# Kernel optimization log

Measured on AMD Instinct MI355X. Metric: run time of the kernel, lower is better.

Reference implementation:

```python
import jax, jax.numpy as jnp
import numpy as np

IMG = 224      # img_size
P = 16         # patch_size
C = 3          # in_chans
K = 100        # n_segments
COMPACT = 10.0 # slic compactness
ITERS = 10     # slic k-means iterations


def _resize_matrix(src, dst):
    # Linear antialiased resize is a linear map; materialize it by resizing identity.
    return jax.image.resize(jnp.eye(src, dtype=jnp.float32), (dst, src),
                            method='linear', antialias=True)


def _slic_labels(img_hwc):
    """Simplified SLIC: grid-initialized k-means in (color, compactness-scaled xy) space."""
    H, W = IMG, IMG
    S = float(np.sqrt(H * W / K))         # superpixel spacing
    ratio = COMPACT / S                   # spatial scaling (SLIC distance weighting)
    yy, xx = jnp.meshgrid(jnp.arange(H, dtype=jnp.float32),
                          jnp.arange(W, dtype=jnp.float32), indexing='ij')
    feat = jnp.concatenate([img_hwc, (yy * ratio)[..., None], (xx * ratio)[..., None]],
                           axis=-1).reshape(H * W, C + 2)  # [HW, 5]
    # grid init of K centers
    gh = int(np.ceil(np.sqrt(K)))
    gw = int(np.ceil(K / gh))
    cy = ((np.arange(gh) + 0.5) * H / gh).astype(np.int32)
    cx = ((np.arange(gw) + 0.5) * W / gw).astype(np.int32)
    idx = (cy[:, None] * W + cx[None, :]).reshape(-1)[:K]
    centers0 = feat[jnp.asarray(idx)]  # [K, 5]

    f2 = jnp.sum(feat * feat, axis=1, keepdims=True)  # [HW,1]

    def dists(centers):
        c2 = jnp.sum(centers * centers, axis=1)  # [K]
        return f2 + c2[None, :] - 2.0 * (feat @ centers.T)  # [HW,K]

    def body(i, centers):
        lbl = jnp.argmin(dists(centers), axis=1)              # [HW]
        oh = jax.nn.one_hot(lbl, K, dtype=feat.dtype)         # [HW,K]
        cnt = oh.sum(0)                                       # [K]
        new = (oh.T @ feat) / jnp.maximum(cnt, 1.0)[:, None]  # [K,5]
        return jnp.where((cnt > 0)[:, None], new, centers)

    centers = jax.lax.fori_loop(0, ITERS, body, centers0)
    return jnp.argmin(dists(centers), axis=1).reshape(H, W)


def _embed_one(img_chw, A):
    img = jnp.transpose(img_chw, (1, 2, 0))                     # [H,W,C]
    labels = jax.lax.stop_gradient(_slic_labels(img))           # [H,W] int
    masks = jax.nn.one_hot(labels, K, dtype=img.dtype, axis=0)  # [K,H,W]
    masked = masks[..., None] * img[None]                       # [K,H,W,C]
    tmp = jnp.einsum('ph,khwc->kpwc', A, masked)                # resize rows
    return jnp.einsum('qw,kpwc->kpqc', A, tmp)                  # [K,P,P,C]


def reference(x):
    B = x.shape[0]
    A = _resize_matrix(IMG, P)
    sp = jax.vmap(lambda im: _embed_one(im, A))(x)  # [B,K,P,P,C]
    # torch: view(B, K*C, P, P)  (raw row-major reinterpret), flatten(2), transpose(1,2)
    out = sp.reshape(B, K * C, P, P).reshape(B, K * C, P * P)
    return jnp.transpose(out, (0, 2, 1))  # [B, P*P, K*C]


def setup_inputs() -> dict:
    key = jax.random.key(0)
    x = jax.random.uniform(key, (8, C, IMG, IMG), dtype=jnp.float32)
    return {"x": x}
```

## Files before the change

### kernel.cpp

```cpp
#include <hip/hip_runtime.h>
#include <math.h>

#define IMGD 224
#define HW 50176
#define NK 100
#define NB 8
#define OUT_PER_B 76800
#define NCHUNK 131
#define MSTR 13
#define PSLAB 640


static __device__ __forceinline__ float ratio_f32() {
  return (float)(10.0 / sqrt(224.0 * 224.0 / 100.0));
}

static __device__ __forceinline__ float dist5s(float f0, float f1, float f2,
                                               float f3, float f4, float fsq,
                                               float c0, float c1, float c2,
                                               float c3, float c4, float q) {
  float dot = __fmul_rn(f0, c0);
  dot = __fmaf_rn(f1, c1, dot);
  dot = __fmaf_rn(f2, c2, dot);
  dot = __fmaf_rn(f3, c3, dot);
  dot = __fmaf_rn(f4, c4, dot);
  return __fsub_rn(__fadd_rn(fsq, q), __fmul_rn(2.0f, dot));
}

static __device__ __forceinline__ float fsq5(float f0, float f1, float f2,
                                             float f3, float f4) {
  float s = __fmul_rn(f0, f0);
  s = __fadd_rn(s, __fmul_rn(f1, f1));
  s = __fadd_rn(s, __fmul_rn(f2, f2));
  s = __fadd_rn(s, __fmul_rn(f3, f3));
  s = __fadd_rn(s, __fmul_rn(f4, f4));
  return s;
}

__global__ void __launch_bounds__(256, 4) iter_kernel(
    const float* __restrict__ x, float* __restrict__ centers,
    const float* __restrict__ c2g, float* __restrict__ partials, int flag,
    float* __restrict__ Ag) {
  __shared__ float4 ck4[NK];
  __shared__ float2 ck2[NK];
  __shared__ unsigned int maskS[2][NK * MSTR];
  __shared__ unsigned short ppkS[2][NK * MSTR];
  __shared__ float4 cval4[2][384];
  __shared__ float  cvalf[2][384];
  __shared__ int cntS[2][128];
  __shared__ int offxS[2][128];
  __shared__ int wtotS[2];
  __shared__ float ubpart[2][12][10];
  __shared__ float ubg[2][12];
  __shared__ unsigned int candm[2][12][4];
  __shared__ float ared[128];
  int bx = blockIdx.x, b = blockIdx.y;
  int tid = threadIdx.x;

  if (bx >= 66) {
    for (int rr = 0; rr < 2; ++rr) {
      int p = 2 * b + rr;
      float cp = (p + 0.5f) * 14.0f - 0.5f;
      if (tid < 128) {
        float xd0 = fabsf(cp - (float)tid) / 14.0f;
        float trip0 = fmaxf(0.0f, 1.0f - xd0);
        float trip1 = 0.0f;
        int t2 = tid + 128;
        if (t2 < IMGD) {
          float xd = fabsf(cp - (float)t2) / 14.0f;
          trip1 = fmaxf(0.0f, 1.0f - xd);
        }
        ared[tid] = trip0 + trip1;
      }
      __syncthreads();
      for (int s = 64; s > 0; s >>= 1) {
        if (tid < s) ared[tid] += ared[tid + s];
        __syncthreads();
      }
      float Zp = ared[0];
      __syncthreads();
      if (tid < IMGD) {
        float xd = fabsf(cp - (float)tid) / 14.0f;
        Ag[p * IMGD + tid] = fmaxf(0.0f, 1.0f - xd) / Zp;
      }
      __syncthreads();
    }
    return;
  }

  int half = tid >> 7;
  int lt = tid & 127;
  int c = 2 * bx + half;
  int start, len;
  if (c < NCHUNK) {
    start = (c < 129) ? c * 384 : 49536 + (c - 129) * 320;
    len   = (c < 129) ? 384 : 320;
  } else {
    start = 0; len = 0;
  }

  const float ratio = ratio_f32();
  const float* x0 = x + (size_t)b * 3 * HW;
  if (flag == 0) {
    if (tid < NK) {
      int gy = tid / 10, gx = tid - 10 * (tid / 10);
      int cy = (int)((gy + 0.5) * 224.0 / 10.0);
      int cx = (int)((gx + 0.5) * 224.0 / 10.0);
      int i = cy * IMGD + cx;
      float c0 = x0[i], c1 = x0[HW + i], c2 = x0[2 * HW + i];
      float c3 = __fmul_rn((float)cy, ratio);
      float c4 = __fmul_rn((float)cx, ratio);
      float s = __fmul_rn(c0, c0);
      s = __fadd_rn(s, __fmul_rn(c1, c1));
      s = __fadd_rn(s, __fmul_rn(c2, c2));
      s = __fadd_rn(s, __fmul_rn(c3, c3));
      s = __fadd_rn(s, __fmul_rn(c4, c4));
      ck4[tid] = make_float4(c0, c1, c2, c3);
      ck2[tid] = make_float2(c4, s);
      if (bx == 0) {
        float* oc = centers + ((size_t)b * NK + tid) * 5;
        oc[0] = c0; oc[1] = c1; oc[2] = c2; oc[3] = c3; oc[4] = c4;
      }
    }
  } else {
    const float* cb = centers + (size_t)b * NK * 5;
    const float* c2b = c2g + (size_t)b * NK;
    if (tid < NK) {
      ck4[tid] = make_float4(cb[tid*5+0], cb[tid*5+1], cb[tid*5+2], cb[tid*5+3]);
      ck2[tid] = make_float2(cb[tid*5+4], c2b[tid]);
    }
  }
  for (int t = lt; t < NK * MSTR; t += 128) maskS[half][t] = 0u;
  if (lt < 48) candm[half][lt >> 2][lt & 3] = 0u;

  float f0[3], f1[3], f2[3], f3[3], f4[3], fq[3];
  bool vld[3];
  for (int r = 0; r < 3; ++r) {
    int t = lt + r * 128;
    vld[r] = (t < len);
    int i = start + (vld[r] ? t : 0);
    int y = i / IMGD, xw = i - y * IMGD;
    f0[r] = x0[i]; f1[r] = x0[HW + i]; f2[r] = x0[2 * HW + i];
    f3[r] = __fmul_rn((float)y, ratio);
    f4[r] = __fmul_rn((float)xw, ratio);
    fq[r] = fsq5(f0[r], f1[r], f2[r], f3[r], f4[r]);
  }
  __syncthreads();

  if (lt < 120) {
    int g = lt / 10, kb = lt - 10 * g;
    int i0 = start + g * 32, i1 = i0 + 31;
    int ymin = i0 / IMGD, ymax = i1 / IMGD;
    int cmin = (ymin == ymax) ? (i0 - ymin * IMGD) : 0;
    int cmax = (ymin == ymax) ? (i1 - ymax * IMGD) : (IMGD - 1);
    float f3mn = __fmul_rn((float)ymin, ratio);
    float f3mx = __fmul_rn((float)ymax, ratio);
    float f4mn = __fmul_rn((float)cmin, ratio);
    float f4mx = __fmul_rn((float)cmax, ratio);
    float mn = 3.4e38f;
    for (int k = kb * 10; k < kb * 10 + 10; ++k) {
      float c3 = ck4[k].w, c4 = ck2[k].x;
      float dy = fmaxf(fabsf(c3 - f3mn), fabsf(c3 - f3mx));
      float dx = fmaxf(fabsf(c4 - f4mn), fabsf(c4 - f4mx));
      mn = fminf(mn, dy * dy + dx * dx + 3.0f);
    }
    ubpart[half][g][kb] = mn;
  }
  __syncthreads();
  if (lt < 12) {
    float mn = ubpart[half][lt][0];
    for (int j = 1; j < 10; ++j) mn = fminf(mn, ubpart[half][lt][j]);
    ubg[half][lt] = mn + 1.0f;
  }
  __syncthreads();
  if (lt < 120) {
    int g = lt / 10, kb = lt - 10 * g;
    int i0 = start + g * 32, i1 = i0 + 31;
    int ymin = i0 / IMGD, ymax = i1 / IMGD;
    int cmin = (ymin == ymax) ? (i0 - ymin * IMGD) : 0;
    int cmax = (ymin == ymax) ? (i1 - ymax * IMGD) : (IMGD - 1);
    float f3mn = __fmul_rn((float)ymin, ratio);
    float f3mx = __fmul_rn((float)ymax, ratio);
    float f4mn = __fmul_rn((float)cmin, ratio);
    float f4mx = __fmul_rn((float)cmax, ratio);
    float lim = ubg[half][g];
    for (int k = kb * 10; k < kb * 10 + 10; ++k) {
      float c3 = ck4[k].w, c4 = ck2[k].x;
      float dy = fmaxf(0.0f, fmaxf(f3mn - c3, c3 - f3mx));
      float dx = fmaxf(0.0f, fmaxf(f4mn - c4, c4 - f4mx));
      if (dy * dy + dx * dx <= lim)
        atomicOr(&candm[half][g][k >> 5], 1u << (k & 31));
    }
  }
  __syncthreads();

  float best[3]; int bk[3];
  for (int r = 0; r < 3; ++r) {
    best[r] = 3.4e38f; bk[r] = 0;
    int t = lt + r * 128;
    int g = (t < 384) ? (t >> 5) : 0;
    for (int w = 0; w < 4; ++w) {
      unsigned int m = candm[half][g][w];
      while (m) {
        int j = __ffs(m) - 1;
        m &= m - 1;
        int k = (w << 5) + j;
        float4 a4 = ck4[k];
        float2 a2 = ck2[k];
        float d = dist5s(f0[r], f1[r], f2[r], f3[r], f4[r], fq[r],
                         a4.x, a4.y, a4.z, a4.w, a2.x, a2.y);
        if (d < best[r]) { best[r] = d; bk[r] = k; }
      }
    }
  }
  for (int r = 0; r < 3; ++r) {
    int t = lt + r * 128;
    if (vld[r]) atomicOr(&maskS[half][bk[r] * MSTR + (t >> 5)], 1u << (t & 31));
  }
  __syncthreads();

  int myCnt = 0;
  if (lt < NK) {
    int s = 0;
    for (int g = 0; g < 12; ++g) {
      ppkS[half][lt * MSTR + g] = (unsigned short)s;
      s += __popc(maskS[half][lt * MSTR + g]);
    }
    myCnt = s;
  }
  cntS[half][lt] = myCnt;
  __syncthreads();

  int v = myCnt;
  for (int d = 1; d < 64; d <<= 1) {
    int u = __shfl_up(v, d, 64);
    if ((tid & 63) >= d) v += u;
  }
  if (lt == 63) wtotS[half] = v;
  __syncthreads();
  if (lt >= 64) v += wtotS[half];
  offxS[half][lt] = v;
  __syncthreads();

  for (int r = 0; r < 3; ++r) {
    int t = lt + r * 128;
    if (vld[r]) {
      int g = t >> 5, j = t & 31;
      unsigned int m = maskS[half][bk[r] * MSTR + g];
      int rank = ppkS[half][bk[r] * MSTR + g] + __popc(m & ((1u << j) - 1u));
      int pos = offxS[half][bk[r]] - cntS[half][bk[r]] + rank;
      cval4[half][pos] = make_float4(f0[r], f1[r], f2[r], f3[r]);
      cvalf[half][pos] = f4[r];
    }
  }
  __syncthreads();

  if (c < NCHUNK && lt < NK) {
    int n = cntS[half][lt];
    int base = offxS[half][lt] - n;
    float s0 = 0.f, s1 = 0.f, s2 = 0.f, s3 = 0.f, s4 = 0.f, s5 = 0.f;
    for (int m = 0; m < n; ++m) {
      float4 vv = cval4[half][base + m];
      float ww = cvalf[half][base + m];
      s0 = __fadd_rn(s0, vv.x);
      s1 = __fadd_rn(s1, vv.y);
      s2 = __fadd_rn(s2, vv.z);
      s3 = __fadd_rn(s3, vv.w);
      s4 = __fadd_rn(s4, ww);
      s5 += 1.0f;
    }
    float* pp = partials + ((size_t)(b * NCHUNK + c)) * PSLAB + lt * 6;
    pp[0] = s0; pp[1] = s1; pp[2] = s2; pp[3] = s3; pp[4] = s4; pp[5] = s5;
  }
}

__global__ void __launch_bounds__(256) combine_update_kernel(
    float* __restrict__ centers, const float* __restrict__ partials,
    float* __restrict__ c2g) {
  __shared__ float st[8 * 6 * NCHUNK];
  __shared__ float sums[8][6];
  __shared__ float newc[8][5];
  int bb = blockIdx.x;
  int tid = threadIdx.x;
  for (int t = tid; t < 8 * 6 * NCHUNK; t += 256) {
    int c = t / 48;
    int rr = t - 48 * c;
    int row = bb * 8 + rr / 6;
    int comp = rr - 6 * (rr / 6);
    int bi = row / 100, ki = row - 100 * bi;
    st[rr * NCHUNK + c] =
        partials[((size_t)(bi * NCHUNK + c)) * PSLAB + ki * 6 + comp];
  }
  __syncthreads();
  if (tid < 48) {
    int row = tid / 6, comp = tid - 6 * (tid / 6);
    const float* rp = st + (row * 6 + comp) * NCHUNK;
    float s = rp[0];
    for (int c = 1; c < NCHUNK; ++c) s = __fadd_rn(s, rp[c]);
    sums[row][comp] = s;
  }
  __syncthreads();
  if (tid < 40) {
    int row = tid / 5, d = tid - 5 * (tid / 5);
    float cntv = sums[row][5];
    float* cc = centers + (size_t)(bb * 8 + row) * 5;
    float v;
    if (cntv > 0.0f) {
      float m = fmaxf(cntv, 1.0f);
      v = __fdiv_rn(sums[row][d], m);
      cc[d] = v;
    } else {
      v = cc[d];
    }
    newc[row][d] = v;
  }
  __syncthreads();
  if (tid < 8) {
    float t0 = __fmul_rn(newc[tid][0], newc[tid][0]);
    t0 = __fadd_rn(t0, __fmul_rn(newc[tid][1], newc[tid][1]));
    t0 = __fadd_rn(t0, __fmul_rn(newc[tid][2], newc[tid][2]));
    t0 = __fadd_rn(t0, __fmul_rn(newc[tid][3], newc[tid][3]));
    t0 = __fadd_rn(t0, __fmul_rn(newc[tid][4], newc[tid][4]));
    c2g[bb * 8 + tid] = t0;
  }
}

__global__ void __launch_bounds__(128, 4) label_kernel(
    const float* __restrict__ x, const float* __restrict__ centers,
    const float* __restrict__ c2g, unsigned char* __restrict__ labels) {
  __shared__ float4 ck4[NK];
  __shared__ float2 ck2[NK];
  __shared__ float ubpart[12][10];
  __shared__ float ubg[12];
  __shared__ unsigned int candm[12][4];
  int c = blockIdx.x, b = blockIdx.y;
  int tid = threadIdx.x;
  int start = (c < 129) ? c * 384 : 49536 + (c - 129) * 320;
  int len   = (c < 129) ? 384 : 320;

  const float ratio = ratio_f32();
  const float* x0 = x + (size_t)b * 3 * HW;
  const float* cb = centers + (size_t)b * NK * 5;
  const float* c2b = c2g + (size_t)b * NK;
  if (tid < NK) {
    ck4[tid] = make_float4(cb[tid*5+0], cb[tid*5+1], cb[tid*5+2], cb[tid*5+3]);
    ck2[tid] = make_float2(cb[tid*5+4], c2b[tid]);
  }
  if (tid < 48) candm[tid >> 2][tid & 3] = 0u;

  float f0[3], f1[3], f2[3], f3[3], f4[3], fq[3];
  int ii[3];
  bool vld[3];
  for (int r = 0; r < 3; ++r) {
    int t = tid + r * 128;
    vld[r] = (t < len);
    int i = start + (vld[r] ? t : 0);
    ii[r] = i;
    int y = i / IMGD, xw = i - y * IMGD;
    f0[r] = x0[i]; f1[r] = x0[HW + i]; f2[r] = x0[2 * HW + i];
    f3[r] = __fmul_rn((float)y, ratio);
    f4[r] = __fmul_rn((float)xw, ratio);
    fq[r] = fsq5(f0[r], f1[r], f2[r], f3[r], f4[r]);
  }
  __syncthreads();

  if (tid < 120) {
    int g = tid / 10, kb = tid - 10 * g;
    int i0 = start + g * 32, i1 = i0 + 31;
    int ymin = i0 / IMGD, ymax = i1 / IMGD;
    int cmin = (ymin == ymax) ? (i0 - ymin * IMGD) : 0;
    int cmax = (ymin == ymax) ? (i1 - ymax * IMGD) : (IMGD - 1);
    float f3mn = __fmul_rn((float)ymin, ratio);
    float f3mx = __fmul_rn((float)ymax, ratio);
    float f4mn = __fmul_rn((float)cmin, ratio);
    float f4mx = __fmul_rn((float)cmax, ratio);
    float mn = 3.4e38f;
    for (int k = kb * 10; k < kb * 10 + 10; ++k) {
      float c3 = ck4[k].w, c4 = ck2[k].x;
      float dy = fmaxf(fabsf(c3 - f3mn), fabsf(c3 - f3mx));
      float dx = fmaxf(fabsf(c4 - f4mn), fabsf(c4 - f4mx));
      mn = fminf(mn, dy * dy + dx * dx + 3.0f);
    }
    ubpart[g][kb] = mn;
  }
  __syncthreads();
  if (tid < 12) {
    float mn = ubpart[tid][0];
    for (int j = 1; j < 10; ++j) mn = fminf(mn, ubpart[tid][j]);
    ubg[tid] = mn + 1.0f;
  }
  __syncthreads();
  if (tid < 120) {
    int g = tid / 10, kb = tid - 10 * g;
    int i0 = start + g * 32, i1 = i0 + 31;
    int ymin = i0 / IMGD, ymax = i1 / IMGD;
    int cmin = (ymin == ymax) ? (i0 - ymin * IMGD) : 0;
    int cmax = (ymin == ymax) ? (i1 - ymax * IMGD) : (IMGD - 1);
    float f3mn = __fmul_rn((float)ymin, ratio);
    float f3mx = __fmul_rn((float)ymax, ratio);
    float f4mn = __fmul_rn((float)cmin, ratio);
    float f4mx = __fmul_rn((float)cmax, ratio);
    float lim = ubg[g];
    for (int k = kb * 10; k < kb * 10 + 10; ++k) {
      float c3 = ck4[k].w, c4 = ck2[k].x;
      float dy = fmaxf(0.0f, fmaxf(f3mn - c3, c3 - f3mx));
      float dx = fmaxf(0.0f, fmaxf(f4mn - c4, c4 - f4mx));
      if (dy * dy + dx * dx <= lim)
        atomicOr(&candm[g][k >> 5], 1u << (k & 31));
    }
  }
  __syncthreads();

  float best[3]; int bk[3];
  for (int r = 0; r < 3; ++r) {
    best[r] = 3.4e38f; bk[r] = 0;
    int t = tid + r * 128;
    int g = (t < 384) ? (t >> 5) : 0;
    for (int w = 0; w < 4; ++w) {
      unsigned int m = candm[g][w];
      while (m) {
        int j = __ffs(m) - 1;
        m &= m - 1;
        int k = (w << 5) + j;
        float4 a4 = ck4[k];
        float2 a2 = ck2[k];
        float d = dist5s(f0[r], f1[r], f2[r], f3[r], f4[r], fq[r],
                         a4.x, a4.y, a4.z, a4.w, a2.x, a2.y);
        if (d < best[r]) { best[r] = d; bk[r] = k; }
      }
    }
  }
  unsigned char* lb = labels + (size_t)b * HW;
  for (int r = 0; r < 3; ++r)
    if (vld[r]) lb[ii[r]] = (unsigned char)bk[r];
}

__global__ void __launch_bounds__(256) embed_kernel(
    const float* __restrict__ x, const unsigned char* __restrict__ labels,
    const float* __restrict__ Ag, float* __restrict__ out) {
  __shared__ float Apv[28];
  __shared__ float Aqw[4][28];
  __shared__ float sk[4][NK * 3];
  int b = blockIdx.y;
  int p = blockIdx.x >> 2;
  int qg = blockIdx.x & 3;
  int q0 = qg * 4;
  int tid = threadIdx.x;

  int h0 = max(0, 14 * p - 7), h1 = min(IMGD - 1, 14 * p + 20);
  int hl = h1 - h0 + 1;
  int w0q[4], w1q[4];
#pragma unroll
  for (int qi = 0; qi < 4; ++qi) {
    int q = q0 + qi;
    w0q[qi] = max(0, 14 * q - 7);
    w1q[qi] = min(IMGD - 1, 14 * q + 20);
  }
  int W0 = w0q[0], W1 = w1q[3];
  int WU = W1 - W0 + 1;

  if (tid < hl) Apv[tid] = Ag[p * IMGD + h0 + tid];
  {
    int t = tid - 64;
    if (t >= 0 && t < 112) {
      int qi = t / 28, dw = t - 28 * qi;
      if (dw <= w1q[qi] - w0q[qi])
        Aqw[qi][dw] = Ag[(q0 + qi) * IMGD + w0q[qi] + dw];
    }
  }
  for (int t = tid; t < 4 * NK * 3; t += 256)
    sk[t / (NK * 3)][t % (NK * 3)] = 0.0f;
  __syncthreads();

  const float* xb = x + (size_t)b * 3 * HW;
  const unsigned char* lb = labels + (size_t)b * HW;
  int n = hl * WU;
  for (int r = 0; r < 8; ++r) {
    int idx = tid + r * 256;
    if (idx >= n) break;
    int dh = idx / WU;
    int dcol = idx - dh * WU;
    int col = W0 + dcol;
    int i = (h0 + dh) * IMGD + col;
    float v0 = xb[i], v1 = xb[HW + i], v2 = xb[2 * HW + i];
    int k = lb[i];
    float ap = Apv[dh];
#pragma unroll
    for (int qi = 0; qi < 4; ++qi) {
      if (col >= w0q[qi] && col <= w1q[qi]) {
        float wgt = ap * Aqw[qi][col - w0q[qi]];
        atomicAdd(&sk[qi][k * 3 + 0], wgt * v0);
        atomicAdd(&sk[qi][k * 3 + 1], wgt * v1);
        atomicAdd(&sk[qi][k * 3 + 2], wgt * v2);
      }
    }
  }
  __syncthreads();

  float* outb = out + (size_t)b * OUT_PER_B;
  for (int t = tid; t < 4 * NK * 3; t += 256) {
    int qi = t / (NK * 3), t3 = t - qi * (NK * 3);
    int k = t3 / 3, cc = t3 - 3 * k;
    int base = p * 48 + (q0 + qi) * 3;
    int f = k * 768 + base + cc;
    outb[(f & 255) * 300 + (f >> 8)] = sk[qi][t3];
  }
}

extern "C" void kernel_launch(void* const* d_in, const int* in_sizes, int n_in,
                              void* d_out, int out_size, void* d_ws, size_t ws_size,
                              hipStream_t stream) {
  const float* x = (const float*)d_in[0];
  float* out = (float*)d_out;
  char* ws = (char*)d_ws;
  float* centers        = (float*)(ws + 16384);
  float* c2g            = (float*)(ws + 49152);
  float* Ag             = (float*)(ws + 65536);
  unsigned char* labels = (unsigned char*)(ws + 98304);
  float* partials       = (float*)(ws + 1703936);

  dim3 ig0(67, NB);
  dim3 ig(66, NB);
  iter_kernel<<<ig0, 256, 0, stream>>>(x, centers, c2g, partials, 0, Ag);
  combine_update_kernel<<<NB * NK / 8, 256, 0, stream>>>(centers, partials, c2g);
  for (int it = 1; it < 10; ++it) {
    iter_kernel<<<ig, 256, 0, stream>>>(x, centers, c2g, partials, 1, Ag);
    combine_update_kernel<<<NB * NK / 8, 256, 0, stream>>>(centers, partials, c2g);
  }
  label_kernel<<<dim3(NCHUNK, NB), 128, 0, stream>>>(x, centers, c2g, labels);
  dim3 egrid(64, NB);
  embed_kernel<<<egrid, 256, 0, stream>>>(x, labels, Ag, out);
}
```

Baseline: 303.7 us.

## Fuse center update into iteration kernels with ping-pong centers and partials buffers

```diff
diff --git a/kernel.cpp b/kernel.cpp
--- a/kernel.cpp
+++ b/kernel.cpp
@@ -38,9 +38,9 @@
 }
 
 __global__ void __launch_bounds__(256, 4) iter_kernel(
-    const float* __restrict__ x, float* __restrict__ centers,
-    const float* __restrict__ c2g, float* __restrict__ partials, int flag,
-    float* __restrict__ Ag) {
+    const float* __restrict__ x, const float* __restrict__ cin,
+    float* __restrict__ cout, const float* __restrict__ pin,
+    float* __restrict__ pout, int flag, float* __restrict__ Ag) {
   __shared__ float4 ck4[NK];
   __shared__ float2 ck2[NK];
   __shared__ unsigned int maskS[2][NK * MSTR];
@@ -118,17 +118,56 @@
       ck4[tid] = make_float4(c0, c1, c2, c3);
       ck2[tid] = make_float2(c4, s);
       if (bx == 0) {
-        float* oc = centers + ((size_t)b * NK + tid) * 5;
+        float* oc = cout + ((size_t)b * NK + tid) * 5;
         oc[0] = c0; oc[1] = c1; oc[2] = c2; oc[3] = c3; oc[4] = c4;
       }
     }
   } else {
-    const float* cb = centers + (size_t)b * NK * 5;
-    const float* c2b = c2g + (size_t)b * NK;
+    float* sumsL  = (float*)&cval4[0][0];
+    float* prevcL = &cvalf[0][0];
+    const float* pb = pin + (size_t)b * NCHUNK * PSLAB;
     if (tid < NK) {
-      ck4[tid] = make_float4(cb[tid*5+0], cb[tid*5+1], cb[tid*5+2], cb[tid*5+3]);
-      ck2[tid] = make_float2(cb[tid*5+4], c2b[tid]);
-    }
+      const float* cp = cin + ((size_t)b * NK + tid) * 5;
+      prevcL[tid * 5 + 0] = cp[0]; prevcL[tid * 5 + 1] = cp[1];
+      prevcL[tid * 5 + 2] = cp[2]; prevcL[tid * 5 + 3] = cp[3];
+      prevcL[tid * 5 + 4] = cp[4];
+    }
+    for (int j = tid; j < NK * 6; j += 256) {
+      const float* q = pb + j;
+      float s = q[0];
+      for (int cc = 1; cc < NCHUNK; ++cc)
+        s = __fadd_rn(s, q[(size_t)cc * PSLAB]);
+      sumsL[j] = s;
+    }
+    __syncthreads();
+    if (tid < NK) {
+      float cnt = sumsL[tid * 6 + 5];
+      float v0, v1, v2, v3, v4;
+      if (cnt > 0.0f) {
+        float m = fmaxf(cnt, 1.0f);
+        v0 = __fdiv_rn(sumsL[tid * 6 + 0], m);
+        v1 = __fdiv_rn(sumsL[tid * 6 + 1], m);
+        v2 = __fdiv_rn(sumsL[tid * 6 + 2], m);
+        v3 = __fdiv_rn(sumsL[tid * 6 + 3], m);
+        v4 = __fdiv_rn(sumsL[tid * 6 + 4], m);
+      } else {
+        v0 = prevcL[tid * 5 + 0]; v1 = prevcL[tid * 5 + 1];
+        v2 = prevcL[tid * 5 + 2]; v3 = prevcL[tid * 5 + 3];
+        v4 = prevcL[tid * 5 + 4];
+      }
+      float t0 = __fmul_rn(v0, v0);
+      t0 = __fadd_rn(t0, __fmul_rn(v1, v1));
+      t0 = __fadd_rn(t0, __fmul_rn(v2, v2));
+      t0 = __fadd_rn(t0, __fmul_rn(v3, v3));
+      t0 = __fadd_rn(t0, __fmul_rn(v4, v4));
+      ck4[tid] = make_float4(v0, v1, v2, v3);
+      ck2[tid] = make_float2(v4, t0);
+      if (bx == 0) {
+        float* oc = cout + ((size_t)b * NK + tid) * 5;
+        oc[0] = v0; oc[1] = v1; oc[2] = v2; oc[3] = v3; oc[4] = v4;
+      }
+    }
+    __syncthreads();
   }
   for (int t = lt; t < NK * MSTR; t += 128) maskS[half][t] = 0u;
   if (lt < 48) candm[half][lt >> 2][lt & 3] = 0u;
@@ -269,90 +308,84 @@
       s4 = __fadd_rn(s4, ww);
       s5 += 1.0f;
     }
-    float* pp = partials + ((size_t)(b * NCHUNK + c)) * PSLAB + lt * 6;
+    float* pp = pout + ((size_t)(b * NCHUNK + c)) * PSLAB + lt * 6;
     pp[0] = s0; pp[1] = s1; pp[2] = s2; pp[3] = s3; pp[4] = s4; pp[5] = s5;
   }
 }
 
-__global__ void __launch_bounds__(256) combine_update_kernel(
-    float* __restrict__ centers, const float* __restrict__ partials,
-    float* __restrict__ c2g) {
-  __shared__ float st[8 * 6 * NCHUNK];
-  __shared__ float sums[8][6];
-  __shared__ float newc[8][5];
-  int bb = blockIdx.x;
-  int tid = threadIdx.x;
-  for (int t = tid; t < 8 * 6 * NCHUNK; t += 256) {
-    int c = t / 48;
-    int rr = t - 48 * c;
-    int row = bb * 8 + rr / 6;
-    int comp = rr - 6 * (rr / 6);
-    int bi = row / 100, ki = row - 100 * bi;
-    st[rr * NCHUNK + c] =
-        partials[((size_t)(bi * NCHUNK + c)) * PSLAB + ki * 6 + comp];
-  }
-  __syncthreads();
-  if (tid < 48) {
-    int row = tid / 6, comp = tid - 6 * (tid / 6);
-    const float* rp = st + (row * 6 + comp) * NCHUNK;
-    float s = rp[0];
-    for (int c = 1; c < NCHUNK; ++c) s = __fadd_rn(s, rp[c]);
-    sums[row][comp] = s;
-  }
-  __syncthreads();
-  if (tid < 40) {
-    int row = tid / 5, d = tid - 5 * (tid / 5);
-    float cntv = sums[row][5];
-    float* cc = centers + (size_t)(bb * 8 + row) * 5;
-    float v;
-    if (cntv > 0.0f) {
-      float m = fmaxf(cntv, 1.0f);
-      v = __fdiv_rn(sums[row][d], m);
-      cc[d] = v;
-    } else {
-      v = cc[d];
-    }
-    newc[row][d] = v;
-  }
-  __syncthreads();
-  if (tid < 8) {
-    float t0 = __fmul_rn(newc[tid][0], newc[tid][0]);
-    t0 = __fadd_rn(t0, __fmul_rn(newc[tid][1], newc[tid][1]));
-    t0 = __fadd_rn(t0, __fmul_rn(newc[tid][2], newc[tid][2]));
-    t0 = __fadd_rn(t0, __fmul_rn(newc[tid][3], newc[tid][3]));
-    t0 = __fadd_rn(t0, __fmul_rn(newc[tid][4], newc[tid][4]));
-    c2g[bb * 8 + tid] = t0;
-  }
-}
-
-__global__ void __launch_bounds__(128, 4) label_kernel(
-    const float* __restrict__ x, const float* __restrict__ centers,
-    const float* __restrict__ c2g, unsigned char* __restrict__ labels) {
+__global__ void __launch_bounds__(256, 4) label_kernel(
+    const float* __restrict__ x, const float* __restrict__ cin,
+    const float* __restrict__ pin, unsigned char* __restrict__ labels) {
   __shared__ float4 ck4[NK];
   __shared__ float2 ck2[NK];
-  __shared__ float ubpart[12][10];
-  __shared__ float ubg[12];
-  __shared__ unsigned int candm[12][4];
-  int c = blockIdx.x, b = blockIdx.y;
+  __shared__ float ubpart[2][12][10];
+  __shared__ float ubg[2][12];
+  __shared__ unsigned int candm[2][12][4];
+  __shared__ float sumsL[NK * 6];
+  __shared__ float prevcL[NK * 5];
+  int bx = blockIdx.x, b = blockIdx.y;
   int tid = threadIdx.x;
-  int start = (c < 129) ? c * 384 : 49536 + (c - 129) * 320;
-  int len   = (c < 129) ? 384 : 320;
+  int half = tid >> 7;
+  int lt = tid & 127;
+  int c = 2 * bx + half;
+  int start, len;
+  if (c < NCHUNK) {
+    start = (c < 129) ? c * 384 : 49536 + (c - 129) * 320;
+    len   = (c < 129) ? 384 : 320;
+  } else {
+    start = 0; len = 0;
+  }
 
   const float ratio = ratio_f32();
   const float* x0 = x + (size_t)b * 3 * HW;
-  const float* cb = centers + (size_t)b * NK * 5;
-  const float* c2b = c2g + (size_t)b * NK;
-  if (tid < NK) {
-    ck4[tid] = make_float4(cb[tid*5+0], cb[tid*5+1], cb[tid*5+2], cb[tid*5+3]);
-    ck2[tid] = make_float2(cb[tid*5+4], c2b[tid]);
-  }
-  if (tid < 48) candm[tid >> 2][tid & 3] = 0u;
+
+  {
+    const float* pb = pin + (size_t)b * NCHUNK * PSLAB;
+    if (tid < NK) {
+      const float* cp = cin + ((size_t)b * NK + tid) * 5;
+      prevcL[tid * 5 + 0] = cp[0]; prevcL[tid * 5 + 1] = cp[1];
+      prevcL[tid * 5 + 2] = cp[2]; prevcL[tid * 5 + 3] = cp[3];
+      prevcL[tid * 5 + 4] = cp[4];
+    }
+    for (int j = tid; j < NK * 6; j += 256) {
+      const float* q = pb + j;
+      float s = q[0];
+      for (int cc = 1; cc < NCHUNK; ++cc)
+        s = __fadd_rn(s, q[(size_t)cc * PSLAB]);
+      sumsL[j] = s;
+    }
+    __syncthreads();
+    if (tid < NK) {
+      float cnt = sumsL[tid * 6 + 5];
+      float v0, v1, v2, v3, v4;
+      if (cnt > 0.0f) {
+        float m = fmaxf(cnt, 1.0f);
+        v0 = __fdiv_rn(sumsL[tid * 6 + 0], m);
+        v1 = __fdiv_rn(sumsL[tid * 6 + 1], m);
+        v2 = __fdiv_rn(sumsL[tid * 6 + 2], m);
+        v3 = __fdiv_rn(sumsL[tid * 6 + 3], m);
+        v4 = __fdiv_rn(sumsL[tid * 6 + 4], m);
+      } else {
+        v0 = prevcL[tid * 5 + 0]; v1 = prevcL[tid * 5 + 1];
+        v2 = prevcL[tid * 5 + 2]; v3 = prevcL[tid * 5 + 3];
+        v4 = prevcL[tid * 5 + 4];
+      }
+      float t0 = __fmul_rn(v0, v0);
+      t0 = __fadd_rn(t0, __fmul_rn(v1, v1));
+      t0 = __fadd_rn(t0, __fmul_rn(v2, v2));
+      t0 = __fadd_rn(t0, __fmul_rn(v3, v3));
+      t0 = __fadd_rn(t0, __fmul_rn(v4, v4));
+      ck4[tid] = make_float4(v0, v1, v2, v3);
+      ck2[tid] = make_float2(v4, t0);
+    }
+  }
+  if (lt < 48) candm[half][lt >> 2][lt & 3] = 0u;
 
   float f0[3], f1[3], f2[3], f3[3], f4[3], fq[3];
   int ii[3];
   bool vld[3];
   for (int r = 0; r < 3; ++r) {
-    int t = tid + r * 128;
+    int t = lt + r * 128;
     vld[r] = (t < len);
     int i = start + (vld[r] ? t : 0);
     ii[r] = i;
@@ -364,8 +397,8 @@
   }
   __syncthreads();
 
-  if (tid < 120) {
-    int g = tid / 10, kb = tid - 10 * g;
+  if (lt < 120) {
+    int g = lt / 10, kb = lt - 10 * g;
     int i0 = start + g * 32, i1 = i0 + 31;
     int ymin = i0 / IMGD, ymax = i1 / IMGD;
     int cmin = (ymin == ymax) ? (i0 - ymin * IMGD) : 0;
@@ -381,17 +414,17 @@
       float dx = fmaxf(fabsf(c4 - f4mn), fabsf(c4 - f4mx));
       mn = fminf(mn, dy * dy + dx * dx + 3.0f);
     }
-    ubpart[g][kb] = mn;
-  }
-  __syncthreads();
-  if (tid < 12) {
-    float mn = ubpart[tid][0];
-    for (int j = 1; j < 10; ++j) mn = fminf(mn, ubpart[tid][j]);
-    ubg[tid] = mn + 1.0f;
-  }
-  __syncthreads();
-  if (tid < 120) {
-    int g = tid / 10, kb = tid - 10 * g;
+    ubpart[half][g][kb] = mn;
+  }
+  __syncthreads();
+  if (lt < 12) {
+    float mn = ubpart[half][lt][0];
+    for (int j = 1; j < 10; ++j) mn = fminf(mn, ubpart[half][lt][j]);
+    ubg[half][lt] = mn + 1.0f;
+  }
+  __syncthreads();
+  if (lt < 120) {
+    int g = lt / 10, kb = lt - 10 * g;
     int i0 = start + g * 32, i1 = i0 + 31;
     int ymin = i0 / IMGD, ymax = i1 / IMGD;
     int cmin = (ymin == ymax) ? (i0 - ymin * IMGD) : 0;
@@ -400,13 +433,13 @@
     float f3mx = __fmul_rn((float)ymax, ratio);
     float f4mn = __fmul_rn((float)cmin, ratio);
     float f4mx = __fmul_rn((float)cmax, ratio);
-    float lim = ubg[g];
+    float lim = ubg[half][g];
     for (int k = kb * 10; k < kb * 10 + 10; ++k) {
       float c3 = ck4[k].w, c4 = ck2[k].x;
       float dy = fmaxf(0.0f, fmaxf(f3mn - c3, c3 - f3mx));
       float dx = fmaxf(0.0f, fmaxf(f4mn - c4, c4 - f4mx));
       if (dy * dy + dx * dx <= lim)
-        atomicOr(&candm[g][k >> 5], 1u << (k & 31));
+        atomicOr(&candm[half][g][k >> 5], 1u << (k & 31));
     }
   }
   __syncthreads();
@@ -414,10 +447,10 @@
   float best[3]; int bk[3];
   for (int r = 0; r < 3; ++r) {
     best[r] = 3.4e38f; bk[r] = 0;
-    int t = tid + r * 128;
+    int t = lt + r * 128;
     int g = (t < 384) ? (t >> 5) : 0;
     for (int w = 0; w < 4; ++w) {
-      unsigned int m = candm[g][w];
+      unsigned int m = candm[half][g][w];
       while (m) {
         int j = __ffs(m) - 1;
         m &= m - 1;
@@ -513,21 +546,23 @@
   const float* x = (const float*)d_in[0];
   float* out = (float*)d_out;
   char* ws = (char*)d_ws;
-  float* centers        = (float*)(ws + 16384);
-  float* c2g            = (float*)(ws + 49152);
+  float* centersA       = (float*)(ws + 16384);
+  float* centersB       = (float*)(ws + 32768);
   float* Ag             = (float*)(ws + 65536);
   unsigned char* labels = (unsigned char*)(ws + 98304);
-  float* partials       = (float*)(ws + 1703936);
+  float* partialsA      = (float*)(ws + 1703936);
+  float* partialsB      = (float*)(ws + 4587520);
+
+  float* C[2] = {centersA, centersB};
+  float* P[2] = {partialsA, partialsB};
 
   dim3 ig0(67, NB);
   dim3 ig(66, NB);
-  iter_kernel<<<ig0, 256, 0, stream>>>(x, centers, c2g, partials, 0, Ag);
-  combine_update_kernel<<<NB * NK / 8, 256, 0, stream>>>(centers, partials, c2g);
-  for (int it = 1; it < 10; ++it) {
-    iter_kernel<<<ig, 256, 0, stream>>>(x, centers, c2g, partials, 1, Ag);
-    combine_update_kernel<<<NB * NK / 8, 256, 0, stream>>>(centers, partials, c2g);
-  }
-  label_kernel<<<dim3(NCHUNK, NB), 128, 0, stream>>>(x, centers, c2g, labels);
+  iter_kernel<<<ig0, 256, 0, stream>>>(x, C[1], C[0], P[1], P[0], 0, Ag);
+  for (int i = 1; i < 10; ++i)
+    iter_kernel<<<ig, 256, 0, stream>>>(x, C[(i - 1) & 1], C[i & 1],
+                                        P[(i - 1) & 1], P[i & 1], 1, Ag);
+  label_kernel<<<ig, 256, 0, stream>>>(x, C[1], P[1], labels);
   dim3 egrid(64, NB);
   embed_kernel<<<egrid, 256, 0, stream>>>(x, labels, Ag, out);
 }
```

Result: slower. 352.8 us (+16.2%).
